# Optimization experiments

Hardware: AMD Instinct MI355X
Metric: run time of the kernel (lower is better)

## Reference

```python
import jax, jax.numpy as jnp
import numpy as np

EPS = 1e-6
NUM_HEADS = 12


def setup_inputs() -> dict:
    key = jax.random.key(0)
    k1, k2, k3, k4 = jax.random.split(key, 4)
    B, N, C = 8, 1024, 768
    x = jax.random.normal(k1, (B, N, C), dtype=jnp.float32)
    # random-walk visitation mask (nonnegative, row 'start_node' weights)
    mask = jax.random.uniform(k2, (N, N), dtype=jnp.float32)
    w_qkv = jax.random.normal(k3, (C, 3 * C), dtype=jnp.float32) * (C ** -0.5)
    w_out = jax.random.normal(k4, (C, C), dtype=jnp.float32) * (C ** -0.5)
    b_out = jnp.zeros((C,), dtype=jnp.float32)
    return {"x": x, "mask": mask, "w_qkv": w_qkv, "w_out": w_out, "b_out": b_out}


def reference(x, mask, w_qkv, w_out, b_out):
    B, N, C = x.shape
    H = NUM_HEADS
    D = C // H
    qkv = x @ w_qkv                      # [B, N, 3C]
    q, k, v = jnp.split(qkv, 3, axis=-1)
    # [B, N, C] -> [B, H, N, D]
    to_heads = lambda t: t.reshape(B, N, H, D).transpose(0, 2, 1, 3)
    q, k, v = to_heads(q), to_heads(k), to_heads(v)
    # feature map: relu + eps
    q = jax.nn.relu(q) + EPS
    k = jax.nn.relu(k) + EPS
    # graph smoothing: (q^T @ mask)^T  ==  einsum over the token axis
    q_graph = jnp.einsum('bhnd,nm->bhmd', q, mask)
    k_graph = jnp.einsum('bhnd,nm->bhmd', k, mask)
    q = q + 0.1 * q_graph
    k = k + 0.1 * k_graph
    # exact linear kernel, masked by random-walk mask
    linear_kernel = jnp.einsum('bhnd,bhmd->bhnm', q, k)   # [B, H, N, N]
    masked_kernel = linear_kernel * mask[None, None]
    z = 1.0 / (masked_kernel.sum(axis=-1, keepdims=True) + EPS)
    out = jnp.einsum('bhnm,bhmd->bhnd', masked_kernel, v) * z
    out = out.transpose(0, 2, 1, 3).reshape(B, N, C)
    return out @ w_out + b_out
```

## Files before the change

kernel.cpp:

```cpp
#include <hip/hip_runtime.h>


typedef unsigned short u16;
typedef unsigned int u32;
typedef __attribute__((ext_vector_type(8))) short short8;
typedef __attribute__((ext_vector_type(4))) float f32x4;

#define MFMA(a, b, c) __builtin_amdgcn_mfma_f32_16x16x32_bf16((a), (b), (c), 0, 0, 0)

__device__ __forceinline__ u16 f2b(float f) {
    unsigned u = __builtin_bit_cast(unsigned, f);
    return (u16)((u + 0x7FFFu + ((u >> 16) & 1u)) >> 16);
}
__device__ __forceinline__ float b2f(u16 h) {
    unsigned u = ((unsigned)h) << 16;
    return __builtin_bit_cast(float, u);
}
__device__ __forceinline__ u32 cvt_pk_bf16(float a, float b) {
    u32 r;
    asm("v_cvt_pk_bf16_f32 %0, %1, %2" : "=v"(r) : "v"(a), "v"(b));
    return r;
}
__device__ __forceinline__ void gl_lds16(const u16* g, u16* l) {
    __builtin_amdgcn_global_load_lds(
        (const __attribute__((address_space(1))) u32*)g,
        (__attribute__((address_space(3))) u32*)l, 16, 0, 0);
}

__global__ __launch_bounds__(256) void k_conv(const float* __restrict__ in,
                                              u16* __restrict__ out, int n) {
    int i = (blockIdx.x * 256 + threadIdx.x) * 4;
    if (i + 3 < n) {
        float4 v = *reinterpret_cast<const float4*>(&in[i]);
        ushort4 o;
        o.x = f2b(v.x); o.y = f2b(v.y); o.z = f2b(v.z); o.w = f2b(v.w);
        *reinterpret_cast<ushort4*>(&out[i]) = o;
    }
}

__global__ __launch_bounds__(256) void k_transconv(const float* __restrict__ in,
                                                   u16* __restrict__ out,
                                                   int R, int Cc, float alpha, float delta) {
    __shared__ float t[32][33];
    const int tx = threadIdx.x & 31, ty = threadIdx.x >> 5;
    const int r0 = blockIdx.y * 32, c0 = blockIdx.x * 32;
#pragma unroll
    for (int k = 0; k < 4; ++k)
        t[ty + 8 * k][tx] = in[(long)(r0 + ty + 8 * k) * Cc + c0 + tx];
    __syncthreads();
#pragma unroll
    for (int k = 0; k < 4; ++k) {
        const int c = c0 + ty + 8 * k, r = r0 + tx;
        float v = t[tx][ty + 8 * k] * alpha + ((r == c) ? delta : 0.f);
        out[(long)c * R + r] = f2b(v);
    }
}

template <int MODE>
__global__ __launch_bounds__(256) void k_gemm(const u16* __restrict__ A,
                                              const u16* __restrict__ Bm,
                                              void* __restrict__ Cv,
                                              const float* __restrict__ bias,
                                              int M, int N, int K,
                                              int lda, int ldb, int ldc,
                                              long boffB, long boffC) {
    __shared__ u16 As[128 * 32];
    __shared__ u16 Bs[128 * 32];
    const int tid = threadIdx.x;
    const int lane = tid & 63, wid = tid >> 6;
    const int lo = lane & 15, hi = lane >> 4;
    const int wr = wid >> 1, wc = wid & 1;
    const int m0 = blockIdx.y * 128, n0 = blockIdx.x * 128;
    const u16* Bz = Bm + (long)blockIdx.z * boffB;

    const int rA = wid * 32 + (lane >> 2);
    const int ck = (lane & 3) * 8;
    const u16* Ag = A + (long)(m0 + rA) * lda + ck;
    const u16* Bg = Bz + (long)(n0 + rA) * ldb + ck;
    u16* AsW = As + (wid * 32) * 32;
    u16* BsW = Bs + (wid * 32) * 32;

    f32x4 acc[4][4] = {};
    for (int k0 = 0; k0 < K; k0 += 32) {
        __syncthreads();
#pragma unroll
        for (int i = 0; i < 2; ++i) {
            gl_lds16(Ag + (long)i * 16 * lda + k0, AsW + i * 16 * 32);
            gl_lds16(Bg + (long)i * 16 * ldb + k0, BsW + i * 16 * 32);
        }
        __syncthreads();
        short8 af[4], bf_[4];
#pragma unroll
        for (int i = 0; i < 4; ++i)
            af[i] = *reinterpret_cast<const short8*>(&As[(wr * 64 + i * 16 + lo) * 32 + hi * 8]);
#pragma unroll
        for (int j = 0; j < 4; ++j)
            bf_[j] = *reinterpret_cast<const short8*>(&Bs[(wc * 64 + j * 16 + lo) * 32 + hi * 8]);
#pragma unroll
        for (int i = 0; i < 4; ++i)
#pragma unroll
            for (int j = 0; j < 4; ++j)
                acc[i][j] = MFMA(af[i], bf_[j], acc[i][j]);
    }

#pragma unroll
    for (int i = 0; i < 4; ++i)
#pragma unroll
        for (int j = 0; j < 4; ++j)
#pragma unroll
            for (int r = 0; r < 4; ++r) {
                const int m = m0 + wr * 64 + i * 16 + hi * 4 + r;
                const int n = n0 + wc * 64 + j * 16 + lo;
                float v = acc[i][j][r];
                if (MODE == 0) {
                    if (m < 1536) v = fmaxf(v, 0.f) + 1e-6f;
                    ((u16*)Cv)[(long)m * ldc + n] = f2b(v);
                } else if (MODE == 1) {
                    u16* Cz = (u16*)Cv + (long)blockIdx.z * boffC;
                    Cz[(long)m * ldc + n] = f2b(v);
                } else {
                    ((float*)Cv)[(long)m * ldc + n] = v + bias[n];
                }
            }
}

__global__ __launch_bounds__(256) void k_attn2(const u16* __restrict__ qks,
                                               const u16* __restrict__ qkvT,
                                               const u16* __restrict__ mb,
                                               u16* __restrict__ attn) {
    __shared__ u16 Ks[2][64][64];
    __shared__ u16 Vt[2][64][64];
    __shared__ u16 Sb[4][16][72];
    __shared__ float Zs[4][2][16];
    const int tid = threadIdx.x, wid = tid >> 6, lane = tid & 63;
    const int lo = lane & 15, hi = lane >> 4;
    const int n0 = blockIdx.x * 128;
    const int bh = blockIdx.y, b = bh / 12, h = bh % 12;
    const long qbase = (long)b * 1024 * 1536;

    short8 aq[2][2];
#pragma unroll
    for (int qg = 0; qg < 2; ++qg)
#pragma unroll
        for (int kd = 0; kd < 2; ++kd)
            aq[qg][kd] = *reinterpret_cast<const short8*>(
                &qks[qbase + (long)(n0 + wid * 32 + qg * 16 + lo) * 1536 + h * 64 +
                     kd * 32 + hi * 8]);

    const u16* gK[2];
    const u16* gV[2];
    int ldsrow[2];
#pragma unroll
    for (int i = 0; i < 2; ++i) {
        const int r = wid * 16 + i * 8 + (lane >> 3);
        const int cs = (lane & 7) ^ (r & 7);
        ldsrow[i] = wid * 16 + i * 8;
        gK[i] = qks + qbase + (long)r * 1536 + 768 + h * 64 + cs * 8;
        gV[i] = qkvT + (long)(1536 + h * 64 + r) * 8192 + (long)b * 1024 + cs * 8;
    }

    const u16* mrow[2];
#pragma unroll
    for (int qg = 0; qg < 2; ++qg)
        mrow[qg] = mb + (long)(n0 + wid * 32 + qg * 16 + lo) * 1024;

    f32x4 oacc[2][4] = {};
    float rsum[2] = {0.f, 0.f};

#pragma unroll
    for (int i = 0; i < 2; ++i) {
        gl_lds16(gK[i], &Ks[0][ldsrow[i]][0]);
        gl_lds16(gV[i], &Vt[0][ldsrow[i]][0]);
    }
    __syncthreads();

    for (int t = 0; t < 16; ++t) {
        const int cur = t & 1;
        if (t < 15) {
            const long m1 = (long)(t + 1) * 64;
#pragma unroll
            for (int i = 0; i < 2; ++i) {
                gl_lds16(gK[i] + m1 * 1536, &Ks[cur ^ 1][ldsrow[i]][0]);
                gl_lds16(gV[i] + m1, &Vt[cur ^ 1][ldsrow[i]][0]);
            }
        }
        short8 kfr[4][2];
#pragma unroll
        for (int jm = 0; jm < 4; ++jm)
#pragma unroll
            for (int kd = 0; kd < 2; ++kd)
                kfr[jm][kd] = *reinterpret_cast<const short8*>(
                    &Ks[cur][jm * 16 + lo][(((kd * 4 + hi) ^ (lo & 7))) * 8]);

#pragma unroll
        for (int qg = 0; qg < 2; ++qg) {
            f32x4 s[4];
#pragma unroll
            for (int jm = 0; jm < 4; ++jm) {
                f32x4 sj = {};
                sj = MFMA(kfr[jm][0], aq[qg][0], sj);
                sj = MFMA(kfr[jm][1], aq[qg][1], sj);
                s[jm] = sj;
            }
#pragma unroll
            for (int jm = 0; jm < 4; ++jm) {
                ushort4 mv = *reinterpret_cast<const ushort4*>(
                    &mrow[qg][t * 64 + jm * 16 + hi * 4]);
                const float p0 = s[jm][0] * b2f(mv.x);
                const float p1 = s[jm][1] * b2f(mv.y);
                const float p2 = s[jm][2] * b2f(mv.z);
                const float p3 = s[jm][3] * b2f(mv.w);
                rsum[qg] += (p0 + p1) + (p2 + p3);
                uint2 packed;
                packed.x = cvt_pk_bf16(p0, p1);
                packed.y = cvt_pk_bf16(p2, p3);
                *reinterpret_cast<uint2*>(&Sb[wid][lo][jm * 16 + hi * 4]) = packed;
            }
#pragma unroll
            for (int km = 0; km < 2; ++km) {
                const short8 pa =
                    *reinterpret_cast<const short8*>(&Sb[wid][lo][km * 32 + hi * 8]);
#pragma unroll
                for (int jd = 0; jd < 4; ++jd) {
                    const short8 vfr = *reinterpret_cast<const short8*>(
                        &Vt[cur][jd * 16 + lo][(((km * 4 + hi) ^ (lo & 7))) * 8]);
                    oacc[qg][jd] = MFMA(pa, vfr, oacc[qg][jd]);
                }
            }
        }
        __syncthreads();
    }

#pragma unroll
    for (int qg = 0; qg < 2; ++qg) {
        float v = rsum[qg];
        v += __shfl_xor(v, 16);
        v += __shfl_xor(v, 32);
        if (hi == 0) Zs[wid][qg][lo] = 1.f / (v + 1e-6f);
    }
    const long obase = (long)(b * 1024) * 768 + h * 64;
#pragma unroll
    for (int qg = 0; qg < 2; ++qg)
#pragma unroll
        for (int jd = 0; jd < 4; ++jd)
#pragma unroll
            for (int r = 0; r < 4; ++r) {
                const int nr = n0 + wid * 32 + qg * 16 + hi * 4 + r;
                attn[obase + (long)nr * 768 + jd * 16 + lo] =
                    f2b(oacc[qg][jd][r] * Zs[wid][qg][hi * 4 + r]);
            }
}


extern "C" void kernel_launch(void* const* d_in, const int* in_sizes, int n_in,
                              void* d_out, int out_size, void* d_ws, size_t ws_size,
                              hipStream_t stream) {
    (void)in_sizes; (void)n_in; (void)out_size; (void)ws_size;
    const float* x     = (const float*)d_in[0];
    const float* mask  = (const float*)d_in[1];
    const float* w_qkv = (const float*)d_in[2];
    const float* w_out = (const float*)d_in[3];
    const float* b_out = (const float*)d_in[4];
    float* out = (float*)d_out;

    u16* ws = (u16*)d_ws;
    u16* xb     = ws;
    u16* wqkvT  = xb + (size_t)8192 * 768;
    u16* mTb    = wqkvT + (size_t)2304 * 768;
    u16* woutT  = mTb + (size_t)1024 * 1024;
    u16* qkvT   = woutT + (size_t)768 * 768;
    u16* qks    = qkvT + (size_t)2304 * 8192;
    u16* attnb  = qks + (size_t)8192 * 1536;
    u16* mbb    = attnb + (size_t)8192 * 768;

    k_conv<<<dim3(6144), dim3(256), 0, stream>>>(x, xb, 8192 * 768);
    k_conv<<<dim3(1024), dim3(256), 0, stream>>>(mask, mbb, 1024 * 1024);
    k_transconv<<<dim3(72, 24), dim3(256), 0, stream>>>(w_qkv, wqkvT, 768, 2304, 1.f, 0.f);
    k_transconv<<<dim3(32, 32), dim3(256), 0, stream>>>(mask, mTb, 1024, 1024, 0.1f, 1.f);
    k_transconv<<<dim3(24, 24), dim3(256), 0, stream>>>(w_out, woutT, 768, 768, 1.f, 0.f);

    k_gemm<0><<<dim3(64, 18, 1), dim3(256), 0, stream>>>(
        wqkvT, xb, qkvT, nullptr, 2304, 8192, 768, 768, 768, 8192, 0, 0);
    k_gemm<1><<<dim3(12, 8, 8), dim3(256), 0, stream>>>(
        mTb, qkvT, qks, nullptr, 1024, 1536, 1024, 1024, 8192, 1536,
        1024L, 1024L * 1536L);
    k_attn2<<<dim3(8, 96), dim3(256), 0, stream>>>(qks, qkvT, mbb, attnb);
    k_gemm<2><<<dim3(6, 64, 1), dim3(256), 0, stream>>>(
        attnb, woutT, out, b_out, 8192, 768, 768, 768, 768, 768, 0, 0);
}
```

Before: 266.0 us.

## Use 256x256 double-buffered GEMM kernel for QKV and mask-smoothing GEMMs

Adds a new GEMM kernel with 512 threads, 256x256 output tiles, K-step 64, and double-buffered LDS, where the next tile's global-to-LDS load is issued before computing the current one. The QKV projection and the graph-smoothing GEMM now use it. The aim is more data reuse per LDS load, fewer barriers per unit of MFMA work, and load latency hidden behind compute. The old kernel is reduced to the output-projection case. Tradeoffs: a 128 KB LDS footprint, high register pressure from 32 accumulators per lane, and far fewer blocks (288 and 192), which may underfill the GPU's compute units.

```diff
diff --git a/kernel.cpp b/kernel.cpp
--- a/kernel.cpp
+++ b/kernel.cpp
@@ -57,13 +57,91 @@
 }
 
 template <int MODE>
+__global__ __launch_bounds__(512, 2) void k_gemm256(const u16* __restrict__ A,
+                                                    const u16* __restrict__ Bm,
+                                                    void* __restrict__ Cv,
+                                                    int M, int N, int K,
+                                                    int lda, int ldb, int ldc,
+                                                    long boffB, long boffC) {
+    __shared__ u16 As[2][256 * 64];
+    __shared__ u16 Bs[2][256 * 64];
+    const int tid = threadIdx.x;
+    const int lane = tid & 63, wid = tid >> 6;
+    const int lo = lane & 15, hi = lane >> 4;
+    const int wr = wid >> 2, wc = wid & 3;
+    const int m0 = blockIdx.y * 256, n0 = blockIdx.x * 256;
+    const u16* Bz = Bm + (long)blockIdx.z * boffB;
+
+    const int srow = wid * 8 + (lane >> 3);
+    const int sch = (lane & 7) * 8;
+    const u16* Ag = A + (long)(m0 + srow) * lda + sch;
+    const u16* Bg = Bz + (long)(n0 + srow) * ldb + sch;
+    const int sldsbase = (wid * 8) * 64;
+
+    f32x4 acc[8][4] = {};
+
+    const int NT = K >> 6;
+#pragma unroll
+    for (int i = 0; i < 4; ++i) {
+        gl_lds16(Ag + (long)i * 64 * lda, &As[0][sldsbase + i * 64 * 64]);
+        gl_lds16(Bg + (long)i * 64 * ldb, &Bs[0][sldsbase + i * 64 * 64]);
+    }
+    __syncthreads();
+
+    for (int t = 0; t < NT; ++t) {
+        const int cur = t & 1;
+        if (t + 1 < NT) {
+            const int k1 = (t + 1) << 6;
+#pragma unroll
+            for (int i = 0; i < 4; ++i) {
+                gl_lds16(Ag + (long)i * 64 * lda + k1, &As[cur ^ 1][sldsbase + i * 64 * 64]);
+                gl_lds16(Bg + (long)i * 64 * ldb + k1, &Bs[cur ^ 1][sldsbase + i * 64 * 64]);
+            }
+        }
+#pragma unroll
+        for (int kk = 0; kk < 2; ++kk) {
+            short8 bfr[4];
+#pragma unroll
+            for (int ni = 0; ni < 4; ++ni)
+                bfr[ni] = *reinterpret_cast<const short8*>(
+                    &Bs[cur][(wc * 64 + ni * 16 + lo) * 64 + kk * 32 + hi * 8]);
+#pragma unroll
+            for (int mi = 0; mi < 8; ++mi) {
+                const short8 afr = *reinterpret_cast<const short8*>(
+                    &As[cur][(wr * 128 + mi * 16 + lo) * 64 + kk * 32 + hi * 8]);
+#pragma unroll
+                for (int ni = 0; ni < 4; ++ni)
+                    acc[mi][ni] = MFMA(afr, bfr[ni], acc[mi][ni]);
+            }
+        }
+        __syncthreads();
+    }
+
+#pragma unroll
+    for (int mi = 0; mi < 8; ++mi)
+#pragma unroll
+        for (int ni = 0; ni < 4; ++ni)
+#pragma unroll
+            for (int r = 0; r < 4; ++r) {
+                const int m = m0 + wr * 128 + mi * 16 + hi * 4 + r;
+                const int n = n0 + wc * 64 + ni * 16 + lo;
+                float v = acc[mi][ni][r];
+                if (MODE == 0) {
+                    if (m < 1536) v = fmaxf(v, 0.f) + 1e-6f;
+                    ((u16*)Cv)[(long)m * ldc + n] = f2b(v);
+                } else {
+                    u16* Cz = (u16*)Cv + (long)blockIdx.z * boffC;
+                    Cz[(long)m * ldc + n] = f2b(v);
+                }
+            }
+}
+
 __global__ __launch_bounds__(256) void k_gemm(const u16* __restrict__ A,
                                               const u16* __restrict__ Bm,
-                                              void* __restrict__ Cv,
+                                              float* __restrict__ Cv,
                                               const float* __restrict__ bias,
                                               int M, int N, int K,
-                                              int lda, int ldb, int ldc,
-                                              long boffB, long boffC) {
+                                              int lda, int ldb, int ldc) {
     __shared__ u16 As[128 * 32];
     __shared__ u16 Bs[128 * 32];
     const int tid = threadIdx.x;
@@ -71,12 +149,11 @@
     const int lo = lane & 15, hi = lane >> 4;
     const int wr = wid >> 1, wc = wid & 1;
     const int m0 = blockIdx.y * 128, n0 = blockIdx.x * 128;
-    const u16* Bz = Bm + (long)blockIdx.z * boffB;
 
     const int rA = wid * 32 + (lane >> 2);
     const int ck = (lane & 3) * 8;
     const u16* Ag = A + (long)(m0 + rA) * lda + ck;
-    const u16* Bg = Bz + (long)(n0 + rA) * ldb + ck;
+    const u16* Bg = Bm + (long)(n0 + rA) * ldb + ck;
     u16* AsW = As + (wid * 32) * 32;
     u16* BsW = Bs + (wid * 32) * 32;
 
@@ -111,16 +188,7 @@
             for (int r = 0; r < 4; ++r) {
                 const int m = m0 + wr * 64 + i * 16 + hi * 4 + r;
                 const int n = n0 + wc * 64 + j * 16 + lo;
-                float v = acc[i][j][r];
-                if (MODE == 0) {
-                    if (m < 1536) v = fmaxf(v, 0.f) + 1e-6f;
-                    ((u16*)Cv)[(long)m * ldc + n] = f2b(v);
-                } else if (MODE == 1) {
-                    u16* Cz = (u16*)Cv + (long)blockIdx.z * boffC;
-                    Cz[(long)m * ldc + n] = f2b(v);
-                } else {
-                    ((float*)Cv)[(long)m * ldc + n] = v + bias[n];
-                }
+                Cv[(long)m * ldc + n] = acc[i][j][r] + bias[n];
             }
 }
 
@@ -279,12 +347,12 @@
     k_transconv<<<dim3(32, 32), dim3(256), 0, stream>>>(mask, mTb, 1024, 1024, 0.1f, 1.f);
     k_transconv<<<dim3(24, 24), dim3(256), 0, stream>>>(w_out, woutT, 768, 768, 1.f, 0.f);
 
-    k_gemm<0><<<dim3(64, 18, 1), dim3(256), 0, stream>>>(
-        wqkvT, xb, qkvT, nullptr, 2304, 8192, 768, 768, 768, 8192, 0, 0);
-    k_gemm<1><<<dim3(12, 8, 8), dim3(256), 0, stream>>>(
-        mTb, qkvT, qks, nullptr, 1024, 1536, 1024, 1024, 8192, 1536,
+    k_gemm256<0><<<dim3(32, 9, 1), dim3(512), 0, stream>>>(
+        wqkvT, xb, qkvT, 2304, 8192, 768, 768, 768, 8192, 0, 0);
+    k_gemm256<1><<<dim3(6, 4, 8), dim3(512), 0, stream>>>(
+        mTb, qkvT, qks, 1024, 1536, 1024, 1024, 8192, 1536,
         1024L, 1024L * 1536L);
     k_attn2<<<dim3(8, 96), dim3(256), 0, stream>>>(qks, qkvT, mbb, attnb);
-    k_gemm<2><<<dim3(6, 64, 1), dim3(256), 0, stream>>>(
-        attnb, woutT, out, b_out, 8192, 768, 768, 768, 768, 768, 0, 0);
-}
+    k_gemm<<<dim3(6, 64, 1), dim3(256), 0, stream>>>(
+        attnb, woutT, out, b_out, 8192, 768, 768, 768, 768, 768);
+}
```

Measured after the change: 294.1 us. +10.6%, slower.
